# Kernel tuning notes

Hardware: AMD Instinct MI355X
Metric: run time of the kernel (lower is better)

The kernel has to match this reference:

```python
import jax, jax.numpy as jnp
import numpy as np
from jax import lax

T_D = 0.7          # condensation radius
T_B = 0.2          # min beta to seed a condensate
FEATURE_LENGTH = 9 # columns of raw features before the prediction block
N_FEAT = 17        # n_ccoords = N_FEAT - 14 = 3
N_EVENTS = 16
POINTS_PER_EVENT = 65536


def setup_inputs() -> dict:
    key = jax.random.key(0)
    N = N_EVENTS * POINTS_PER_EVENT
    # uniform [0,1): betas in [0,1), ccoords in the unit cube -> realistic clustering
    x = jax.random.uniform(key, (N, N_FEAT), dtype=jnp.float32)
    row_splits = (jnp.arange(N_EVENTS + 1) * POINTS_PER_EVENT).astype(jnp.int32)
    return {"x": x, "row_splits": row_splits}


def _build_condensates(ccoords, betas, radius, min_beta):
    """Greedy NMS-like condensation, vectorized over events.
    ccoords: [E, P, C] float; betas: [E, P] float.
    Returns asso [E,P] int32 (index of assigned condensate, -1 = noise) and
    iscond [E,P] bool (condensation point flags).
    """
    E, P, _ = ccoords.shape
    r2 = radius * radius

    def masked_beta(asso):
        return jnp.where(asso < 0, betas, -1.0)

    def cond_fn(state):
        asso, _ = state
        return jnp.any(jnp.max(masked_beta(asso), axis=1) >= min_beta)

    def body_fn(state):
        asso, iscond = state
        mb = masked_beta(asso)                     # [E,P]
        ref = jnp.argmax(mb, axis=1)               # [E] highest-beta unassigned point
        valid = jnp.take_along_axis(mb, ref[:, None], axis=1)[:, 0] >= min_beta  # [E]
        refc = jnp.take_along_axis(ccoords, ref[:, None, None], axis=1)          # [E,1,C]
        distsq = jnp.sum((ccoords - refc) ** 2, axis=-1)                          # [E,P]
        assign = (asso < 0) & (distsq <= r2) & valid[:, None]
        asso = jnp.where(assign, ref[:, None].astype(jnp.int32), asso)
        newcond = (jnp.arange(P)[None, :] == ref[:, None]) & valid[:, None]
        return asso, iscond | newcond

    asso0 = jnp.full((E, P), -1, dtype=jnp.int32)
    iscond0 = jnp.zeros((E, P), dtype=jnp.bool_)
    return lax.while_loop(cond_fn, body_fn, (asso0, iscond0))


def reference(x, row_splits):
    E = row_splits.shape[0] - 1
    N, F = x.shape
    P = N // E  # uniform events (RaggedConstructTensor equivalent for equal splits)
    n_ccoords = F - 14
    x_pred = x[:, FEATURE_LENGTH:]
    n_pred = x_pred.shape[-1]
    betas = x_pred[:, 0].reshape(E, P)
    ccoords = x_pred[:, n_pred - n_ccoords:].reshape(E, P, n_ccoords)

    asso, iscond = _build_condensates(ccoords, betas, T_D, T_B)

    ncond = jnp.sum(iscond, axis=1).astype(jnp.int32)  # condensates per event
    out_row_splits = jnp.concatenate(
        [jnp.zeros((1,), jnp.int32), jnp.cumsum(ncond).astype(jnp.int32)])
    # jit-safe equivalent of dout = x[iscond > 0]: zero-mask non-condensates
    mask = iscond.reshape(-1, 1).astype(x.dtype)
    dout = x * mask  # [N, F], rows of non-condensates are zero
    return dout, out_row_splits
```

## Files before the change

kernel.cpp:

```cpp
#include <hip/hip_runtime.h>

typedef unsigned long long u64;
typedef unsigned int u32;

static constexpr int NF = 17;
static constexpr int BCOL = 9;
static constexpr int CCOL = 14;
static constexpr int CONDCAP = 1024;
static constexpr int RPB = 512;
static constexpr int LCAP = 7168;
static constexpr int FT = 1024;

#define T_B_F ((float)0.2)
#define R2_F  ((float)(0.7*0.7))

__device__ __forceinline__ u64 kmax(u64 a, u64 b){ return a > b ? a : b; }

__device__ __forceinline__ u64 shfl_down_u64(u64 v, int off){
    u32 lo = (u32)v, hi = (u32)(v >> 32);
    lo = __shfl_down(lo, off, 64);
    hi = __shfl_down(hi, off, 64);
    return ((u64)hi << 32) | lo;
}

__device__ __forceinline__ u64 shfl_u64(u64 v, int lane){
    u32 lo = (u32)v, hi = (u32)(v >> 32);
    lo = __shfl(lo, lane, 64);
    hi = __shfl(hi, lane, 64);
    return ((u64)hi << 32) | lo;
}

__device__ __forceinline__ u64 waveReduceMax(u64 k){
    #pragma unroll
    for (int off = 32; off > 0; off >>= 1){
        u64 o = shfl_down_u64(k, off);
        if (o > k) k = o;
    }
    return k;
}

__device__ __forceinline__ float dist2(float cx, float cy, float cz,
                                       float rx, float ry, float rz){
    #pragma clang fp contract(off)
    float dx = cx - rx, dy = cy - ry, dz = cz - rz;
    float sx = dx * dx, sy = dy * dy, sz = dz * dz;
    return (sx + sy) + sz;
}

__device__ __forceinline__ u64 makeKey(float beta, u32 idx){
    return ((u64)__float_as_uint(beta) << 32) | (u64)(0xFFFFFFFFu - idx);
}

__global__ void k_init(u32* ws){
    int t = threadIdx.x;
    if (t < 1024) ws[t] = 0;
}

__global__ __launch_bounds__(512) void k_filter(
    const float4* __restrict__ x4, float4* __restrict__ out4,
    u64* __restrict__ argmax0, int* __restrict__ cnt0,
    float4* __restrict__ cA, int* __restrict__ iA,
    int P, int chunksPerEvent)
{
    __shared__ float lds[RPB * NF];
    __shared__ int swc[8], swb[8], sbase;
    __shared__ u64 sred[8];

    int e = blockIdx.x / chunksPerEvent;
    int chunk = blockIdx.x % chunksPerEvent;
    int rowStart = chunk * RPB;
    size_t tile4 = (size_t)blockIdx.x * (RPB * NF / 4);

    float4* lds4 = (float4*)lds;
    const int N4 = RPB * NF / 4;
    float4 z = make_float4(0.f, 0.f, 0.f, 0.f);
    for (int i = threadIdx.x; i < N4; i += 512){
        lds4[i] = x4[tile4 + i];
        out4[tile4 + i] = z;
    }
    __syncthreads();

    int tid = threadIdx.x, lid = tid & 63, wid = tid >> 6;
    float be = lds[tid*NF+BCOL];
    float cx = lds[tid*NF+CCOL], cy = lds[tid*NF+CCOL+1], cz = lds[tid*NF+CCOL+2];
    bool kp = (be >= T_B_F);
    u64 bal = __ballot(kp);
    int wcnt = __popcll(bal);
    u64 lk = kp ? makeKey(be, (u32)(rowStart + tid)) : 0;
    u64 kw = waveReduceMax(lk);
    if (lid == 0){ swc[wid] = wcnt; sred[wid] = kw; }
    __syncthreads();
    if (tid == 0){
        int tot = 0;
        for (int w = 0; w < 8; w++){ swb[w] = tot; tot += swc[w]; }
        sbase = tot ? atomicAdd(&cnt0[e], tot) : 0;
        u64 m = sred[0];
        for (int i = 1; i < 8; i++) m = kmax(m, sred[i]);
        if (m) atomicMax(&argmax0[e], m);
    }
    __syncthreads();
    if (kp){
        int pos = sbase + swb[wid] + __popcll(bal & ((1ull << lid) - 1));
        size_t eoff = (size_t)e * P;
        cA[eoff + pos] = make_float4(cx, cy, cz, be);
        iA[eoff + pos] = rowStart + tid;
    }
}

__global__ __launch_bounds__(1024) void k_finish(
    const float* __restrict__ x,
    float4* cA, int* iA, float4* cB, int* iB,
    const u64* __restrict__ argmax0, const int* __restrict__ cnt0,
    int* __restrict__ ncond, int* __restrict__ done,
    float* __restrict__ out, int P, int E)
{
    __shared__ u64 skey[LCAP];
    __shared__ float sx[LCAP], sy[LCAP], sz[LCAP];
    __shared__ u64 sred[16];
    __shared__ int condL[CONDCAP];
    __shared__ int scnt, snc;
    __shared__ u64 skeyb;
    __shared__ float srefc[3];

    int e = blockIdx.x;
    int tid = threadIdx.x, lid = tid & 63, wid = tid >> 6;
    int n = cnt0[e];
    u64 key = argmax0[e];
    float4* cIn = cA + (size_t)e * P; int* iIn = iA + (size_t)e * P;
    float4* cOut = cB + (size_t)e * P; int* iOut = iB + (size_t)e * P;

    if (tid == 0) snc = 0;
    __syncthreads();

    while (n > LCAP){
        float betaRef = __uint_as_float((u32)(key >> 32));
        if (!(betaRef >= T_B_F)) break;
        u32 refIdx = 0xFFFFFFFFu - (u32)(key & 0xFFFFFFFFu);
        if (tid == 0){
            if (snc < CONDCAP) condL[snc] = (int)refIdx;
            snc++;
            size_t rbase = ((size_t)e * P + refIdx) * NF;
            srefc[0] = x[rbase + CCOL];
            srefc[1] = x[rbase + CCOL + 1];
            srefc[2] = x[rbase + CCOL + 2];
            scnt = 0;
        }
        __syncthreads();
        float rx = srefc[0], ry = srefc[1], rz = srefc[2];
        u64 localKey = 0;
        for (int i = tid; i < n; i += FT){
            float4 cc = cIn[i]; int idx = iIn[i];
            float d2 = dist2(cc.x, cc.y, cc.z, rx, ry, rz);
            bool keep = !(d2 <= R2_F);
            u64 bal = __ballot(keep);
            int cw = __popcll(bal);
            int b_ = 0;
            if (lid == 0) b_ = cw ? atomicAdd(&scnt, cw) : 0;
            b_ = __shfl(b_, 0, 64);
            if (keep){
                int pos = b_ + __popcll(bal & ((1ull << lid) - 1));
                cOut[pos] = cc; iOut[pos] = idx;
                localKey = kmax(localKey, makeKey(cc.w, (u32)idx));
            }
        }
        u64 kw = waveReduceMax(localKey);
        if (lid == 0) sred[wid] = kw;
        __syncthreads();
        if (tid == 0){
            u64 m = 0;
            for (int i = 0; i < 16; i++) m = kmax(m, sred[i]);
            skeyb = m;
        }
        __syncthreads();
        key = skeyb; n = scnt;
        { float4* t = cIn; cIn = cOut; cOut = t; }
        { int* t = iIn; iIn = iOut; iOut = t; }
        __syncthreads();
    }

    float betaRef0 = __uint_as_float((u32)(key >> 32));
    if (betaRef0 >= T_B_F && n > 0){
        for (int i = tid; i < n; i += FT){
            float4 cc = cIn[i]; int idx = iIn[i];
            skey[i] = makeKey(cc.w, (u32)idx);
            sx[i] = cc.x; sy[i] = cc.y; sz[i] = cc.z;
        }
        __syncthreads();

        if (wid == 0){
            int snc_l = snc;
            int mp = -1;
            while (true){
                float betaRef = __uint_as_float((u32)(key >> 32));
                if (!(betaRef >= T_B_F)) break;
                u32 refIdx = 0xFFFFFFFFu - (u32)(key & 0xFFFFFFFFu);
                if (lid == 0 && snc_l < CONDCAP) condL[snc_l] = (int)refIdx;
                snc_l++;
                float rx, ry, rz;
                if (mp >= 0){ rx = sx[mp]; ry = sy[mp]; rz = sz[mp]; }
                else {
                    size_t rbase = ((size_t)e * P + refIdx) * NF;
                    rx = x[rbase + CCOL]; ry = x[rbase + CCOL + 1]; rz = x[rbase + CCOL + 2];
                }
                u64 bk = 0; int bp = -1;
                int alive = 0;
                for (int i0 = 0; i0 < n; i0 += 64){
                    int i = i0 + lid;
                    bool inb = i < n;
                    int ii = inb ? i : 0;
                    u64 k = skey[ii];
                    float xx = sx[ii], yy = sy[ii], zz = sz[ii];
                    float d2 = dist2(xx, yy, zz, rx, ry, rz);
                    bool keep = inb && !(d2 <= R2_F);
                    u64 b = __ballot(keep);
                    if (keep){
                        int pos = alive + __popcll(b & ((1ull << lid) - 1));
                        skey[pos] = k; sx[pos] = xx; sy[pos] = yy; sz[pos] = zz;
                        if (k > bk){ bk = k; bp = pos; }
                    }
                    alive += __popcll(b);
                }
                #pragma unroll
                for (int off = 32; off > 0; off >>= 1){
                    u64 ok = shfl_down_u64(bk, off);
                    int op = __shfl_down(bp, off, 64);
                    if (ok > bk){ bk = ok; bp = op; }
                }
                key = shfl_u64(bk, 0);
                mp = __shfl(bp, 0, 64);
                n = alive;
            }
            if (lid == 0) snc = snc_l;
        }
    }
    __syncthreads();

    int ncT = snc;
    int ncc = ncT > CONDCAP ? CONDCAP : ncT;
    for (int i = tid; i < ncc * NF; i += FT){
        int j = i / NF, f = i - j * NF;
        int row = condL[j];
        size_t base = ((size_t)e * P + row) * NF;
        out[base + f] = x[base + f];
    }
    if (tid == 0){
        ncond[e] = ncT;
        __threadfence();
        int r = atomicAdd(done, 1);
        if (r == E - 1){
            size_t ob = (size_t)E * P * NF;
            int s = 0;
            out[ob] = 0.0f;
            for (int i = 0; i < E; i++){
                s += atomicAdd(&ncond[i], 0);
                out[ob + i + 1] = (float)s;
            }
        }
    }
}

extern "C" void kernel_launch(void* const* d_in, const int* in_sizes, int n_in,
                              void* d_out, int out_size, void* d_ws, size_t ws_size,
                              hipStream_t stream) {
    const float* x = (const float*)d_in[0];
    int N = in_sizes[0] / NF;
    int E = in_sizes[1] - 1;
    int P = N / E;
    float* out = (float*)d_out;
    char* ws = (char*)d_ws;

    u64* argmax = (u64*)ws;
    int* cnt    = (int*)(ws + 1024);
    int* ncond  = (int*)(ws + 2048);
    int* done   = (int*)(ws + 2560);
    size_t listOff = 32768;
    size_t listElems = (size_t)E * P;
    float4* cA = (float4*)(ws + listOff);
    float4* cB = (float4*)(ws + listOff + listElems * 16);
    int* iA = (int*)(ws + listOff + listElems * 32);
    int* iB = (int*)(ws + listOff + listElems * 36);

    k_init<<<1, 1024, 0, stream>>>((u32*)ws);

    int chunksPerEvent = P / RPB;
    k_filter<<<E * chunksPerEvent, 512, 0, stream>>>(
        (const float4*)x, (float4*)out, argmax, cnt, cA, iA, P, chunksPerEvent);

    k_finish<<<E, 1024, 0, stream>>>(
        x, cA, iA, cB, iB, argmax, cnt, ncond, done, out, P, E);
}
```

Baseline: 228.0 us.

## Batch multiple condensate selections per compaction pass using per-wave top-4 candidates

Drops the shared-memory tail phase and makes the block-wide compaction loop select several condensates per pass. Each wave keeps a top-4 of surviving keys. Wave 0 bitonic-sorts the 64 candidates and greedily accepts those above a safety threshold that are not suppressed by earlier accepted ones. The next pass then removes points within radius of all accepted references at once, with KB-way unrolled loads. This aims to cut the number of full-array global passes and barriers. The cost is extra per-point distance checks against multiple references, and correctness relies on the tau bound.

```diff
diff --git a/kernel.cpp b/kernel.cpp
--- a/kernel.cpp
+++ b/kernel.cpp
@@ -8,8 +8,8 @@
 static constexpr int CCOL = 14;
 static constexpr int CONDCAP = 1024;
 static constexpr int RPB = 512;
-static constexpr int LCAP = 7168;
 static constexpr int FT = 1024;
+static constexpr int KB = 8;
 
 #define T_B_F ((float)0.2)
 #define R2_F  ((float)(0.7*0.7))
@@ -27,6 +27,13 @@
     u32 lo = (u32)v, hi = (u32)(v >> 32);
     lo = __shfl(lo, lane, 64);
     hi = __shfl(hi, lane, 64);
+    return ((u64)hi << 32) | lo;
+}
+
+__device__ __forceinline__ u64 shfl_xor_u64(u64 v, int mask){
+    u32 lo = (u32)v, hi = (u32)(v >> 32);
+    lo = __shfl_xor(lo, mask, 64);
+    hi = __shfl_xor(hi, mask, 64);
     return ((u64)hi << 32) | lo;
 }
 
@@ -114,124 +121,148 @@
     int* __restrict__ ncond, int* __restrict__ done,
     float* __restrict__ out, int P, int E)
 {
-    __shared__ u64 skey[LCAP];
-    __shared__ float sx[LCAP], sy[LCAP], sz[LCAP];
-    __shared__ u64 sred[16];
+    __shared__ u64 wtopk[64];
+    __shared__ int wtopp[64];
+    __shared__ float refX[64], refY[64], refZ[64];
     __shared__ int condL[CONDCAP];
-    __shared__ int scnt, snc;
-    __shared__ u64 skeyb;
-    __shared__ float srefc[3];
+    __shared__ int scnt, snc, snr;
 
     int e = blockIdx.x;
     int tid = threadIdx.x, lid = tid & 63, wid = tid >> 6;
     int n = cnt0[e];
-    u64 key = argmax0[e];
+    u64 key0 = argmax0[e];
     float4* cIn = cA + (size_t)e * P; int* iIn = iA + (size_t)e * P;
     float4* cOut = cB + (size_t)e * P; int* iOut = iB + (size_t)e * P;
 
-    if (tid == 0) snc = 0;
-    __syncthreads();
-
-    while (n > LCAP){
-        float betaRef = __uint_as_float((u32)(key >> 32));
-        if (!(betaRef >= T_B_F)) break;
-        u32 refIdx = 0xFFFFFFFFu - (u32)(key & 0xFFFFFFFFu);
-        if (tid == 0){
-            if (snc < CONDCAP) condL[snc] = (int)refIdx;
-            snc++;
+    if (tid == 0){
+        snc = 0; scnt = 0; snr = 0;
+        float b0 = __uint_as_float((u32)(key0 >> 32));
+        if (n > 0 && b0 >= T_B_F){
+            u32 refIdx = 0xFFFFFFFFu - (u32)key0;
+            condL[0] = (int)refIdx; snc = 1; snr = 1;
             size_t rbase = ((size_t)e * P + refIdx) * NF;
-            srefc[0] = x[rbase + CCOL];
-            srefc[1] = x[rbase + CCOL + 1];
-            srefc[2] = x[rbase + CCOL + 2];
-            scnt = 0;
+            refX[0] = x[rbase + CCOL];
+            refY[0] = x[rbase + CCOL + 1];
+            refZ[0] = x[rbase + CCOL + 2];
+        }
+    }
+    __syncthreads();
+
+    while (snr > 0){
+        int nr = snr;
+
+        u64 k4a=0,k4b=0,k4c=0,k4d=0; int p4a=0,p4b=0,p4c=0,p4d=0;
+        for (int base = 0; base < n; base += FT * KB){
+            float4 cc[KB]; int ixv[KB]; bool kp[KB]; u64 bal[KB];
+            #pragma unroll
+            for (int k = 0; k < KB; k++){
+                int i = base + tid + k * FT;
+                bool inb = i < n; int ii = inb ? i : 0;
+                cc[k] = cIn[ii]; ixv[k] = iIn[ii];
+                kp[k] = inb;
+            }
+            #pragma unroll
+            for (int k = 0; k < KB; k++){
+                if (kp[k]){
+                    for (int r = 0; r < nr; r++){
+                        if (dist2(cc[k].x, cc[k].y, cc[k].z,
+                                  refX[r], refY[r], refZ[r]) <= R2_F){ kp[k] = false; break; }
+                    }
+                }
+            }
+            int wcnt = 0;
+            #pragma unroll
+            for (int k = 0; k < KB; k++){ bal[k] = __ballot(kp[k]); wcnt += __popcll(bal[k]); }
+            int wb = 0;
+            if (lid == 0) wb = wcnt ? atomicAdd(&scnt, wcnt) : 0;
+            wb = __shfl(wb, 0, 64);
+            u64 lm = (1ull << lid) - 1;
+            #pragma unroll
+            for (int k = 0; k < KB; k++){
+                if (kp[k]){
+                    int pos = wb + __popcll(bal[k] & lm);
+                    cOut[pos] = cc[k]; iOut[pos] = ixv[k];
+                    u64 kk = makeKey(cc[k].w, (u32)ixv[k]);
+                    if (kk > k4d){
+                        if (kk > k4a){ k4d=k4c;p4d=p4c; k4c=k4b;p4c=p4b; k4b=k4a;p4b=p4a; k4a=kk;p4a=pos; }
+                        else if (kk > k4b){ k4d=k4c;p4d=p4c; k4c=k4b;p4c=p4b; k4b=kk;p4b=pos; }
+                        else if (kk > k4c){ k4d=k4c;p4d=p4c; k4c=kk;p4c=pos; }
+                        else { k4d=kk; p4d=pos; }
+                    }
+                }
+                wb += __popcll(bal[k]);
+            }
+        }
+        {
+            u64 excl = ~0ull;
+            #pragma unroll
+            for (int j = 0; j < 4; j++){
+                u64 lk = 0; int lp = 0;
+                if (k4a < excl && k4a > lk){ lk = k4a; lp = p4a; }
+                if (k4b < excl && k4b > lk){ lk = k4b; lp = p4b; }
+                if (k4c < excl && k4c > lk){ lk = k4c; lp = p4c; }
+                if (k4d < excl && k4d > lk){ lk = k4d; lp = p4d; }
+                #pragma unroll
+                for (int off = 32; off > 0; off >>= 1){
+                    u64 ok = shfl_down_u64(lk, off);
+                    int op = __shfl_down(lp, off, 64);
+                    if (ok > lk){ lk = ok; lp = op; }
+                }
+                lk = shfl_u64(lk, 0); lp = __shfl(lp, 0, 64);
+                if (lid == 0){ wtopk[wid*4 + j] = lk; wtopp[wid*4 + j] = lp; }
+                excl = lk;
+            }
         }
         __syncthreads();
-        float rx = srefc[0], ry = srefc[1], rz = srefc[2];
-        u64 localKey = 0;
-        for (int i = tid; i < n; i += FT){
-            float4 cc = cIn[i]; int idx = iIn[i];
-            float d2 = dist2(cc.x, cc.y, cc.z, rx, ry, rz);
-            bool keep = !(d2 <= R2_F);
-            u64 bal = __ballot(keep);
-            int cw = __popcll(bal);
-            int b_ = 0;
-            if (lid == 0) b_ = cw ? atomicAdd(&scnt, cw) : 0;
-            b_ = __shfl(b_, 0, 64);
-            if (keep){
-                int pos = b_ + __popcll(bal & ((1ull << lid) - 1));
-                cOut[pos] = cc; iOut[pos] = idx;
-                localKey = kmax(localKey, makeKey(cc.w, (u32)idx));
-            }
-        }
-        u64 kw = waveReduceMax(localKey);
-        if (lid == 0) sred[wid] = kw;
-        __syncthreads();
-        if (tid == 0){
-            u64 m = 0;
-            for (int i = 0; i < 16; i++) m = kmax(m, sred[i]);
-            skeyb = m;
-        }
-        __syncthreads();
-        key = skeyb; n = scnt;
+        n = scnt;
         { float4* t = cIn; cIn = cOut; cOut = t; }
         { int* t = iIn; iIn = iOut; iOut = t; }
+        if (n == 0) break;
+
+        if (wid == 0){
+            u64 key = wtopk[lid]; int pos = wtopp[lid];
+            u64 tt = (lid < 16) ? wtopk[lid*4 + 3] : 0;
+            u64 tau = waveReduceMax(tt); tau = shfl_u64(tau, 0);
+            float cx = 0.f, cy = 0.f, cz = 0.f;
+            if (key){ float4 c = cIn[pos]; cx = c.x; cy = c.y; cz = c.z; }
+            #pragma unroll
+            for (int bs = 2; bs <= 64; bs <<= 1){
+                #pragma unroll
+                for (int bj = bs >> 1; bj > 0; bj >>= 1){
+                    u64 ok = shfl_xor_u64(key, bj);
+                    float ox = __shfl_xor(cx, bj, 64);
+                    float oy = __shfl_xor(cy, bj, 64);
+                    float oz = __shfl_xor(cz, bj, 64);
+                    bool lower = (lid & bj) == 0;
+                    bool segDesc = (lid & bs) == 0;
+                    bool takeOther = segDesc ? (lower ? (ok > key) : (ok < key))
+                                             : (lower ? (ok < key) : (ok > key));
+                    if (takeOther){ key = ok; cx = ox; cy = oy; cz = oz; }
+                }
+            }
+            int killed = (key == 0) ? 1 : 0;
+            int nrr = 0;
+            int sb = snc;
+            for (int j = 0; j < 64; j++){
+                u64 kj = shfl_u64(key, j);
+                if (kj == 0 || kj <= tau) break;
+                int kb = __shfl(killed, j, 64);
+                if (!kb){
+                    float xj = __shfl(cx, j, 64);
+                    float yj = __shfl(cy, j, 64);
+                    float zj = __shfl(cz, j, 64);
+                    if (lid == 0){
+                        refX[nrr] = xj; refY[nrr] = yj; refZ[nrr] = zj;
+                        int s = sb + nrr;
+                        if (s < CONDCAP) condL[s] = (int)(0xFFFFFFFFu - (u32)kj);
+                    }
+                    nrr++;
+                    if (dist2(cx, cy, cz, xj, yj, zj) <= R2_F) killed = 1;
+                }
+            }
+            if (lid == 0){ snr = nrr; snc = sb + nrr; scnt = 0; }
+        }
         __syncthreads();
-    }
-
-    float betaRef0 = __uint_as_float((u32)(key >> 32));
-    if (betaRef0 >= T_B_F && n > 0){
-        for (int i = tid; i < n; i += FT){
-            float4 cc = cIn[i]; int idx = iIn[i];
-            skey[i] = makeKey(cc.w, (u32)idx);
-            sx[i] = cc.x; sy[i] = cc.y; sz[i] = cc.z;
-        }
-        __syncthreads();
-
-        if (wid == 0){
-            int snc_l = snc;
-            int mp = -1;
-            while (true){
-                float betaRef = __uint_as_float((u32)(key >> 32));
-                if (!(betaRef >= T_B_F)) break;
-                u32 refIdx = 0xFFFFFFFFu - (u32)(key & 0xFFFFFFFFu);
-                if (lid == 0 && snc_l < CONDCAP) condL[snc_l] = (int)refIdx;
-                snc_l++;
-                float rx, ry, rz;
-                if (mp >= 0){ rx = sx[mp]; ry = sy[mp]; rz = sz[mp]; }
-                else {
-                    size_t rbase = ((size_t)e * P + refIdx) * NF;
-                    rx = x[rbase + CCOL]; ry = x[rbase + CCOL + 1]; rz = x[rbase + CCOL + 2];
-                }
-                u64 bk = 0; int bp = -1;
-                int alive = 0;
-                for (int i0 = 0; i0 < n; i0 += 64){
-                    int i = i0 + lid;
-                    bool inb = i < n;
-                    int ii = inb ? i : 0;
-                    u64 k = skey[ii];
-                    float xx = sx[ii], yy = sy[ii], zz = sz[ii];
-                    float d2 = dist2(xx, yy, zz, rx, ry, rz);
-                    bool keep = inb && !(d2 <= R2_F);
-                    u64 b = __ballot(keep);
-                    if (keep){
-                        int pos = alive + __popcll(b & ((1ull << lid) - 1));
-                        skey[pos] = k; sx[pos] = xx; sy[pos] = yy; sz[pos] = zz;
-                        if (k > bk){ bk = k; bp = pos; }
-                    }
-                    alive += __popcll(b);
-                }
-                #pragma unroll
-                for (int off = 32; off > 0; off >>= 1){
-                    u64 ok = shfl_down_u64(bk, off);
-                    int op = __shfl_down(bp, off, 64);
-                    if (ok > bk){ bk = ok; bp = op; }
-                }
-                key = shfl_u64(bk, 0);
-                mp = __shfl(bp, 0, 64);
-                n = alive;
-            }
-            if (lid == 0) snc = snc_l;
-        }
     }
     __syncthreads();
 
```

After: 243.7 us. +6.9%, slower.

## Pre-resolve high-beta condensates, then bulk-kill assigned points in parallel

Applied to the files above, without the earlier changes.

Points with beta at or above a threshold (0.93) are gathered into a small candidate list. A per-event kernel runs the greedy condensation on that list first. This is exact because no lower-beta point can become a reference before all higher-beta candidates are handled. A new wide-grid kernel then removes every point within radius of those references across many blocks and recomputes the per-event argmax. The serial per-event finish loop therefore starts from a much smaller list. The cost is two extra launches and capped candidate and reference counts. Events that exceed those caps fall back to the original path.

```diff
diff --git a/kernel.cpp b/kernel.cpp
--- a/kernel.cpp
+++ b/kernel.cpp
@@ -6,13 +6,17 @@
 static constexpr int NF = 17;
 static constexpr int BCOL = 9;
 static constexpr int CCOL = 14;
-static constexpr int CONDCAP = 1024;
+static constexpr int CONDCAP = 256;
+static constexpr int REFCAP = 256;
+static constexpr int CANDCAP = 6144;
 static constexpr int RPB = 512;
+static constexpr int FT = 1024;
+static constexpr int KB = 8;
 static constexpr int LCAP = 7168;
-static constexpr int FT = 1024;
-
-#define T_B_F ((float)0.2)
-#define R2_F  ((float)(0.7*0.7))
+
+#define T_B_F  ((float)0.2)
+#define R2_F   ((float)(0.7*0.7))
+#define TAU0_F ((float)0.93)
 
 __device__ __forceinline__ u64 kmax(u64 a, u64 b){ return a > b ? a : b; }
 
@@ -37,6 +41,15 @@
         if (o > k) k = o;
     }
     return k;
+}
+
+__device__ __forceinline__ void waveReduceMaxPair(u64 &k, int &p){
+    #pragma unroll
+    for (int off = 32; off > 0; off >>= 1){
+        u64 ok = shfl_down_u64(k, off);
+        int op = __shfl_down(p, off, 64);
+        if (ok > k){ k = ok; p = op; }
+    }
 }
 
 __device__ __forceinline__ float dist2(float cx, float cy, float cz,
@@ -58,13 +71,13 @@
 
 __global__ __launch_bounds__(512) void k_filter(
     const float4* __restrict__ x4, float4* __restrict__ out4,
-    u64* __restrict__ argmax0, int* __restrict__ cnt0,
-    float4* __restrict__ cA, int* __restrict__ iA,
+    int* __restrict__ cnt0, float4* __restrict__ cA, int* __restrict__ iA,
+    int* __restrict__ candCnt, int* __restrict__ candI,
     int P, int chunksPerEvent)
 {
     __shared__ float lds[RPB * NF];
     __shared__ int swc[8], swb[8], sbase;
-    __shared__ u64 sred[8];
+    __shared__ int swc2[8], swb2[8], sbase2;
 
     int e = blockIdx.x / chunksPerEvent;
     int chunk = blockIdx.x % chunksPerEvent;
@@ -84,34 +97,189 @@
     float be = lds[tid*NF+BCOL];
     float cx = lds[tid*NF+CCOL], cy = lds[tid*NF+CCOL+1], cz = lds[tid*NF+CCOL+2];
     bool kp = (be >= T_B_F);
-    u64 bal = __ballot(kp);
-    int wcnt = __popcll(bal);
-    u64 lk = kp ? makeKey(be, (u32)(rowStart + tid)) : 0;
-    u64 kw = waveReduceMax(lk);
-    if (lid == 0){ swc[wid] = wcnt; sred[wid] = kw; }
+    bool cd = (be >= TAU0_F);
+    u64 bal  = __ballot(kp);
+    u64 bal2 = __ballot(cd);
+    if (lid == 0){ swc[wid] = __popcll(bal); swc2[wid] = __popcll(bal2); }
     __syncthreads();
     if (tid == 0){
-        int tot = 0;
-        for (int w = 0; w < 8; w++){ swb[w] = tot; tot += swc[w]; }
-        sbase = tot ? atomicAdd(&cnt0[e], tot) : 0;
-        u64 m = sred[0];
-        for (int i = 1; i < 8; i++) m = kmax(m, sred[i]);
-        if (m) atomicMax(&argmax0[e], m);
-    }
-    __syncthreads();
+        int tot = 0, tot2 = 0;
+        for (int w = 0; w < 8; w++){
+            swb[w] = tot;  tot  += swc[w];
+            swb2[w] = tot2; tot2 += swc2[w];
+        }
+        sbase  = tot  ? atomicAdd(&cnt0[e], tot)     : 0;
+        sbase2 = tot2 ? atomicAdd(&candCnt[e], tot2) : 0;
+    }
+    __syncthreads();
+    u64 lm = (1ull << lid) - 1;
     if (kp){
-        int pos = sbase + swb[wid] + __popcll(bal & ((1ull << lid) - 1));
+        int pos = sbase + swb[wid] + __popcll(bal & lm);
         size_t eoff = (size_t)e * P;
         cA[eoff + pos] = make_float4(cx, cy, cz, be);
         iA[eoff + pos] = rowStart + tid;
     }
-}
-
-__global__ __launch_bounds__(1024) void k_finish(
+    if (cd){
+        int pos = sbase2 + swb2[wid] + __popcll(bal2 & lm);
+        if (pos < CANDCAP) candI[e * CANDCAP + pos] = rowStart + tid;
+    }
+}
+
+__global__ __launch_bounds__(1024) void k_resolve(
+    const float* __restrict__ x, const int* __restrict__ candCnt,
+    const int* __restrict__ candI, int* __restrict__ nrefs,
+    int* __restrict__ condlist, float* __restrict__ refXg,
+    float* __restrict__ refYg, float* __restrict__ refZg, int P)
+{
+    __shared__ u64 skey[CANDCAP];
+    __shared__ float sx[CANDCAP], sy[CANDCAP], sz[CANDCAP];
+    __shared__ u64 wk[16]; __shared__ int wp[16];
+    __shared__ float rfx[REFCAP], rfy[REFCAP], rfz[REFCAP];
+    __shared__ int rci[REFCAP];
+    __shared__ int snr;
+
+    int e = blockIdx.x;
+    int tid = threadIdx.x, lid = tid & 63, wid = tid >> 6;
+    int m = candCnt[e];
+    if (m > CANDCAP || m == 0){ if (tid == 0) nrefs[e] = 0; return; }
+
+    u64 bk = 0; int bp = 0;
+    for (int i = tid; i < m; i += FT){
+        int idx = candI[e * CANDCAP + i];
+        size_t rb = ((size_t)e * P + idx) * NF;
+        float be = x[rb + BCOL];
+        u64 k = makeKey(be, (u32)idx);
+        skey[i] = k;
+        sx[i] = x[rb + CCOL]; sy[i] = x[rb + CCOL + 1]; sz[i] = x[rb + CCOL + 2];
+        if (k > bk){ bk = k; bp = i; }
+    }
+    waveReduceMaxPair(bk, bp);
+    if (lid == 0){ wk[wid] = bk; wp[wid] = bp; }
+    __syncthreads();
+
+    if (wid == 0){
+        u64 key = (lid < 16) ? wk[lid] : 0;
+        int mp  = (lid < 16) ? wp[lid] : 0;
+        waveReduceMaxPair(key, mp);
+        key = shfl_u64(key, 0); mp = __shfl(mp, 0, 64);
+
+        int n = m, nr = 0;
+        while (key){
+            if (nr == REFCAP) break;
+            float rx = sx[mp], ry = sy[mp], rz = sz[mp];
+            if (lid == 0){
+                rfx[nr] = rx; rfy[nr] = ry; rfz[nr] = rz;
+                rci[nr] = (int)(0xFFFFFFFFu - (u32)key);
+            }
+            nr++;
+            u64 nk = 0; int np = -1; int alive = 0;
+            for (int i0 = 0; i0 < n; i0 += 64){
+                int i = i0 + lid;
+                bool inb = i < n;
+                int ii = inb ? i : 0;
+                u64 k2 = skey[ii];
+                float xx = sx[ii], yy = sy[ii], zz = sz[ii];
+                bool keep = inb && !(dist2(xx, yy, zz, rx, ry, rz) <= R2_F);
+                u64 b = __ballot(keep);
+                if (keep){
+                    int pos = alive + __popcll(b & ((1ull << lid) - 1));
+                    skey[pos] = k2; sx[pos] = xx; sy[pos] = yy; sz[pos] = zz;
+                    if (k2 > nk){ nk = k2; np = pos; }
+                }
+                alive += __popcll(b);
+            }
+            waveReduceMaxPair(nk, np);
+            key = shfl_u64(nk, 0); mp = __shfl(np, 0, 64);
+            n = alive;
+        }
+        if (lid == 0) snr = nr;
+    }
+    __syncthreads();
+    int nr = snr;
+    for (int i = tid; i < nr; i += FT){
+        refXg[e*REFCAP + i] = rfx[i];
+        refYg[e*REFCAP + i] = rfy[i];
+        refZg[e*REFCAP + i] = rfz[i];
+        condlist[e*CONDCAP + i] = rci[i];
+    }
+    if (tid == 0) nrefs[e] = nr;
+}
+
+__global__ __launch_bounds__(256) void k_kill(
+    const float4* __restrict__ cA, const int* __restrict__ iA,
+    float4* __restrict__ cB, int* __restrict__ iB,
+    const int* __restrict__ cnt0, int* __restrict__ cnt1,
+    u64* __restrict__ argmax1, const int* __restrict__ nrefs,
+    const float* __restrict__ refXg, const float* __restrict__ refYg,
+    const float* __restrict__ refZg, int P, int bpe)
+{
+    __shared__ float rfx[REFCAP], rfy[REFCAP], rfz[REFCAP];
+    __shared__ int swc[4], swb[4], sbase;
+    __shared__ u64 sred[4];
+
+    int e = blockIdx.x / bpe;
+    int c = blockIdx.x % bpe;
+    int n = cnt0[e];
+    if (c * 256 >= n) return;
+    int nr = nrefs[e];
+    for (int i = threadIdx.x; i < nr; i += 256){
+        rfx[i] = refXg[e*REFCAP + i];
+        rfy[i] = refYg[e*REFCAP + i];
+        rfz[i] = refZg[e*REFCAP + i];
+    }
+    __syncthreads();
+
+    int tid = threadIdx.x, lid = tid & 63, wid = tid >> 6;
+    size_t eoff = (size_t)e * P;
+    int stride = bpe * 256;
+
+    float4 cc[KB]; int ixv[KB]; bool kp[KB]; u64 bal[KB];
+    int wcnt = 0; u64 lk = 0;
+    #pragma unroll
+    for (int k = 0; k < KB; k++){
+        int i = c * 256 + tid + k * stride;
+        bool inb = i < n;
+        int ii = inb ? i : 0;
+        cc[k] = cA[eoff + ii]; ixv[k] = iA[eoff + ii];
+        bool alive = inb;
+        for (int r = 0; r < nr; r++){
+            if (alive && dist2(cc[k].x, cc[k].y, cc[k].z, rfx[r], rfy[r], rfz[r]) <= R2_F)
+                alive = false;
+        }
+        kp[k] = alive;
+        bal[k] = __ballot(alive);
+        wcnt += __popcll(bal[k]);
+        if (alive) lk = kmax(lk, makeKey(cc[k].w, (u32)ixv[k]));
+    }
+    u64 kw = waveReduceMax(lk);
+    if (lid == 0){ swc[wid] = wcnt; sred[wid] = kw; }
+    __syncthreads();
+    if (tid == 0){
+        int tot = 0;
+        for (int w = 0; w < 4; w++){ swb[w] = tot; tot += swc[w]; }
+        sbase = tot ? atomicAdd(&cnt1[e], tot) : 0;
+        u64 mm = kmax(kmax(sred[0], sred[1]), kmax(sred[2], sred[3]));
+        if (mm) atomicMax(&argmax1[e], mm);
+    }
+    __syncthreads();
+    int pos = sbase + swb[wid];
+    u64 lm = (1ull << lid) - 1;
+    #pragma unroll
+    for (int k = 0; k < KB; k++){
+        if (kp[k]){
+            int p_ = pos + __popcll(bal[k] & lm);
+            cB[eoff + p_] = cc[k]; iB[eoff + p_] = ixv[k];
+        }
+        pos += __popcll(bal[k]);
+    }
+}
+
+__global__ __launch_bounds__(1024) void k_finish2(
     const float* __restrict__ x,
-    float4* cA, int* iA, float4* cB, int* iB,
-    const u64* __restrict__ argmax0, const int* __restrict__ cnt0,
-    int* __restrict__ ncond, int* __restrict__ done,
+    float4* cB, int* iB, float4* cA, int* iA,
+    const u64* __restrict__ argmax1, const int* __restrict__ cnt1,
+    const int* __restrict__ nrefs, int* __restrict__ ncond,
+    const int* __restrict__ condlistG, int* __restrict__ done,
     float* __restrict__ out, int P, int E)
 {
     __shared__ u64 skey[LCAP];
@@ -124,12 +292,14 @@
 
     int e = blockIdx.x;
     int tid = threadIdx.x, lid = tid & 63, wid = tid >> 6;
-    int n = cnt0[e];
-    u64 key = argmax0[e];
-    float4* cIn = cA + (size_t)e * P; int* iIn = iA + (size_t)e * P;
-    float4* cOut = cB + (size_t)e * P; int* iOut = iB + (size_t)e * P;
-
-    if (tid == 0) snc = 0;
+    int n = cnt1[e];
+    u64 key = argmax1[e];
+    float4* cIn = cB + (size_t)e * P; int* iIn = iB + (size_t)e * P;
+    float4* cOut = cA + (size_t)e * P; int* iOut = iA + (size_t)e * P;
+
+    int nr0 = nrefs[e];
+    for (int i = tid; i < nr0; i += FT) condL[i] = condlistG[e*CONDCAP + i];
+    if (tid == 0) snc = nr0;
     __syncthreads();
 
     while (n > LCAP){
@@ -220,12 +390,7 @@
                     }
                     alive += __popcll(b);
                 }
-                #pragma unroll
-                for (int off = 32; off > 0; off >>= 1){
-                    u64 ok = shfl_down_u64(bk, off);
-                    int op = __shfl_down(bp, off, 64);
-                    if (ok > bk){ bk = ok; bp = op; }
-                }
+                waveReduceMaxPair(bk, bp);
                 key = shfl_u64(bk, 0);
                 mp = __shfl(bp, 0, 64);
                 n = alive;
@@ -252,7 +417,7 @@
             int s = 0;
             out[ob] = 0.0f;
             for (int i = 0; i < E; i++){
-                s += atomicAdd(&ncond[i], 0);
+                s += atomicAdd((int*)&ncond[i], 0);
                 out[ob + i + 1] = (float)s;
             }
         }
@@ -269,23 +434,38 @@
     float* out = (float*)d_out;
     char* ws = (char*)d_ws;
 
-    u64* argmax = (u64*)ws;
-    int* cnt    = (int*)(ws + 1024);
-    int* ncond  = (int*)(ws + 2048);
-    int* done   = (int*)(ws + 2560);
-    size_t listOff = 32768;
+    u64* argmax1 = (u64*)ws;
+    int* cnt0    = (int*)(ws + 1024);
+    int* cnt1    = (int*)(ws + 1280);
+    int* candCnt = (int*)(ws + 1536);
+    int* nrefs   = (int*)(ws + 1792);
+    int* ncond   = (int*)(ws + 2048);
+    int* done    = (int*)(ws + 2304);
+    int* condlist= (int*)(ws + 4096);
+    float* refXg = (float*)(ws + 20480);
+    float* refYg = (float*)(ws + 36864);
+    float* refZg = (float*)(ws + 53248);
+    size_t listOff = 69632;
     size_t listElems = (size_t)E * P;
     float4* cA = (float4*)(ws + listOff);
     float4* cB = (float4*)(ws + listOff + listElems * 16);
     int* iA = (int*)(ws + listOff + listElems * 32);
     int* iB = (int*)(ws + listOff + listElems * 36);
+    int* candI = iB;
 
     k_init<<<1, 1024, 0, stream>>>((u32*)ws);
 
     int chunksPerEvent = P / RPB;
     k_filter<<<E * chunksPerEvent, 512, 0, stream>>>(
-        (const float4*)x, (float4*)out, argmax, cnt, cA, iA, P, chunksPerEvent);
-
-    k_finish<<<E, 1024, 0, stream>>>(
-        x, cA, iA, cB, iB, argmax, cnt, ncond, done, out, P, E);
-}
+        (const float4*)x, (float4*)out, cnt0, cA, iA, candCnt, candI, P, chunksPerEvent);
+
+    k_resolve<<<E, 1024, 0, stream>>>(
+        x, candCnt, candI, nrefs, condlist, refXg, refYg, refZg, P);
+
+    int bpe = 32;
+    k_kill<<<E * bpe, 256, 0, stream>>>(
+        cA, iA, cB, iB, cnt0, cnt1, argmax1, nrefs, refXg, refYg, refZg, P, bpe);
+
+    k_finish2<<<E, 1024, 0, stream>>>(
+        x, cB, iB, cA, iA, argmax1, cnt1, nrefs, ncond, condlist, done, out, P, E);
+}
```

After: 196.6 us. 1.16x faster.
